# Kernel tuning notes

Hardware: AMD Instinct MI355X
Metric: run time of the kernel (lower is better)

Reference implementation:

```python
import jax, jax.numpy as jnp
import numpy as np

H = 2048          # hidden_size
I = 768           # moe_intermediate_size
E = 64            # num_experts
TOP_K = 8         # num_experts_per_tok (norm_topk_prob=True)
B, S = 1, 1024


def setup_inputs() -> dict:
    key = jax.random.key(0)
    ks = jax.random.split(key, 5)
    scale = 0.02
    return {
        "hidden_states": jax.random.normal(ks[0], (B, S, H), dtype=jnp.float32),
        "W_router": jax.random.normal(ks[1], (H, E), dtype=jnp.float32) * scale,
        "W_gate": jax.random.normal(ks[2], (E, H, I), dtype=jnp.float32) * scale,
        "W_up": jax.random.normal(ks[3], (E, H, I), dtype=jnp.float32) * scale,
        "W_down": jax.random.normal(ks[4], (E, I, H), dtype=jnp.float32) * scale,
    }


def reference(hidden_states, W_router, W_gate, W_up, W_down):
    b, s, h = hidden_states.shape
    x = hidden_states.reshape(-1, h)                      # [T, H]

    # --- Qwen3MoeTopKRouter: linear gate -> fp32 softmax -> top-k -> renorm ---
    logits = x @ W_router                                 # [T, E]
    probs = jax.nn.softmax(logits.astype(jnp.float32), axis=-1)
    top_w, top_idx = jax.lax.top_k(probs, TOP_K)          # [T, K]
    top_w = top_w / jnp.sum(top_w, axis=-1, keepdims=True)  # norm_topk_prob
    top_w = top_w.astype(x.dtype)

    # combine weights per (token, expert): zero if expert not selected
    comb = jnp.sum(jax.nn.one_hot(top_idx, E, dtype=x.dtype) * top_w[..., None], axis=1)  # [T, E]

    # --- per-expert SwiGLU MLP: down(silu(gate(x)) * up(x)), dense-masked ---
    g = jnp.einsum('th,ehi->eti', x, W_gate)              # [E, T, I]
    u = jnp.einsum('th,ehi->eti', x, W_up)                # [E, T, I]
    hmid = jax.nn.silu(g) * u                             # [E, T, I]
    # fold combine weight into the intermediate to avoid an [E, T, H] buffer
    hmid = hmid * comb.T[:, :, None]                      # [E, T, I]
    out = jnp.einsum('eti,eih->th', hmid, W_down)         # [T, H]

    return out.reshape(b, s, h)
```

## Files before the change

### kernel.cpp

```cpp
#include <hip/hip_runtime.h>
#include <hip/hip_bf16.h>

#define H_DIM 2048
#define I_DIM 768
#define NEXP 64
#define TOPK 8
#define NTOK 1024
#define BM 256
#define BKS 32

typedef float f32x4 __attribute__((ext_vector_type(4)));
typedef unsigned int u32x4 __attribute__((ext_vector_type(4)));
typedef unsigned int u32x2 __attribute__((ext_vector_type(2)));
typedef short bf16v8 __attribute__((ext_vector_type(8)));
typedef unsigned short u16x8 __attribute__((ext_vector_type(8)));
typedef unsigned int u32;

#define NTLOAD __builtin_nontemporal_load

#define WS_NEEDED 50954752ull

__device__ inline unsigned short f2bf(float f) {
    union { float f; u32 u; } v; v.f = f;
    u32 r = (v.u + 0x7FFFu + ((v.u >> 16) & 1u)) >> 16;
    return (unsigned short)r;
}
__device__ inline u32 pack2(float a, float b) {
    return (u32)f2bf(a) | ((u32)f2bf(b) << 16);
}

__global__ void zero_kernel(float4* p, int n4) {
    int i = blockIdx.x * blockDim.x + threadIdx.x;
    if (i < n4) p[i] = (float4){0.f, 0.f, 0.f, 0.f};
}

__global__ __launch_bounds__(512) void router_kernel(
    const float* __restrict__ x, const float* __restrict__ Wr,
    int* __restrict__ topk_idx, float* __restrict__ topk_w,
    ushort4* __restrict__ xbf)
{
    const int t   = blockIdx.x;
    const int tid = threadIdx.x;
    const int lane = tid & 63;
    const int wv   = tid >> 6;
    __shared__ float xs[H_DIM];
    __shared__ float red[8][64];

    const float* xrow = x + (size_t)t * H_DIM;
    {
        const float4* src = (const float4*)xrow;
        float4 v = src[tid];
        ((float4*)xs)[tid] = v;
        ushort4 o;
        o.x = f2bf(v.x); o.y = f2bf(v.y); o.z = f2bf(v.z); o.w = f2bf(v.w);
        xbf[(size_t)t * (H_DIM / 4) + tid] = o;
    }
    __syncthreads();

    float acc = 0.f;
    const int h0 = wv * 256;
    #pragma unroll 8
    for (int h = h0; h < h0 + 256; ++h) acc += xs[h] * Wr[(size_t)h * NEXP + lane];
    red[wv][lane] = acc;
    __syncthreads();

    if (tid < 64) {
        const int e = tid;
        float logit = ((red[0][e] + red[1][e]) + (red[2][e] + red[3][e]))
                    + ((red[4][e] + red[5][e]) + (red[6][e] + red[7][e]));

        float m = logit;
        #pragma unroll
        for (int o = 32; o > 0; o >>= 1) m = fmaxf(m, __shfl_xor(m, o));
        float p = __expf(logit - m);
        float s = p;
        #pragma unroll
        for (int o = 32; o > 0; o >>= 1) s += __shfl_xor(s, o);
        float prob = p / s;

        float myp = prob;
        float kw[TOPK]; int kid[TOPK]; float wsum = 0.f;
        #pragma unroll
        for (int k = 0; k < TOPK; ++k) {
            float v = myp; int bi = e;
            #pragma unroll
            for (int o = 32; o > 0; o >>= 1) {
                float ov = __shfl_xor(v, o);
                int   oi = __shfl_xor(bi, o);
                if (ov > v || (ov == v && oi < bi)) { v = ov; bi = oi; }
            }
            kw[k] = v; kid[k] = bi; wsum += v;
            if (e == bi) myp = -1.f;
        }
        if (e == 0) {
            float inv = 1.f / wsum;
            #pragma unroll
            for (int k = 0; k < TOPK; ++k) {
                topk_idx[t * TOPK + k] = kid[k];
                topk_w[t * TOPK + k]   = kw[k] * inv;
            }
        }
    }
}

__global__ __launch_bounds__(64) void listbuild_kernel(
    const int* __restrict__ topk_idx, const float* __restrict__ topk_w,
    int* __restrict__ counts, int* __restrict__ lists, float* __restrict__ wlist,
    int* __restrict__ invmap)
{
    const int e = blockIdx.x;
    const int lane = threadIdx.x;
    int n = 0;
    for (int base = 0; base < NTOK * TOPK; base += 64) {
        int s = base + lane;
        int idx = topk_idx[s];
        bool match = (idx == e);
        unsigned long long mask = __ballot(match);
        int pre = __popcll(mask & ((1ull << lane) - 1ull));
        if (match) {
            lists[e * NTOK + n + pre] = s >> 3;
            wlist[e * NTOK + n + pre] = topk_w[s];
            invmap[s] = n + pre;
        }
        n += __popcll(mask);
    }
    if (lane == 0) counts[e] = n;
}

__global__ __launch_bounds__(64) void scan_kernel(
    const int* __restrict__ counts, int* __restrict__ offsets)
{
    int e = threadIdx.x;
    int v = counts[e];
    int xacc = v;
    #pragma unroll
    for (int o = 1; o < 64; o <<= 1) {
        int y = __shfl_up(xacc, o);
        if (e >= o) xacc += y;
    }
    offsets[e] = xacc - v;
}

#define MFMA_BF16 __builtin_amdgcn_mfma_f32_16x16x32_bf16
#define LGKM0()  asm volatile("s_waitcnt lgkmcnt(0)" ::: "memory")
#define RAWBAR() __builtin_amdgcn_s_barrier()

__global__ __launch_bounds__(512) void gateup_kernel(
    const unsigned short* __restrict__ xbf,
    const float* __restrict__ Wg, const float* __restrict__ Wu,
    const int* __restrict__ counts, const int* __restrict__ offsets,
    const int* __restrict__ lists, const float* __restrict__ wlist,
    unsigned short* __restrict__ hmid)
{
    const int b  = blockIdx.x;
    const int wg = (b & 7) * 192 + (b >> 3);
    const int itile = wg % 24;
    const int e     = wg / 24;

    const int count = counts[e];
    if (count == 0) return;
    const int off = offsets[e];
    const int i0 = itile * 32;

    __shared__ unsigned short Alds[2][BM][40];
    __shared__ u32 Bgl[2][32 * 20];
    __shared__ u32 Bul[2][32 * 20];

    const int tid  = threadIdx.x;
    const int lane = tid & 63;
    const int wid  = tid >> 6;
    const int wm   = wid >> 1, wn = wid & 1;
    const int kb   = lane >> 4;
    const int l15  = lane & 15;

    const int ar = tid >> 1;
    const int ah = (tid & 1) * 16;
    const int bnn  = tid & 31;
    const int bkq  = (tid >> 5) & 7;
    const int bmat = tid >> 8;
    const float* WB = (bmat ? Wu : Wg) + (size_t)e * H_DIM * I_DIM + i0 + bnn;
    const int key4w = 4 * ((bnn >> 3) & 3);
    const int bwoff = bnn * 20 + ((2 * bkq) ^ key4w);
    const int brn   = wn * 16 + l15;
    const int key4r = 4 * ((brn >> 3) & 3);

    for (int mstart = 0; mstart < count; mstart += BM) {
        const int pr = mstart + ar;
        const bool aact = pr < count;
        const unsigned short* xrow = xbf + (size_t)(aact ? lists[e * NTOK + pr] : 0) * H_DIM + ah;
        const bool mact = (mstart + wm * 64) < count;

        f32x4 accg[4], accu[4];
        #pragma unroll
        for (int i = 0; i < 4; ++i) {
            accg[i] = (f32x4){0.f, 0.f, 0.f, 0.f};
            accu[i] = (f32x4){0.f, 0.f, 0.f, 0.f};
        }

        u32x4 aA0, aA1, aB0, aB1;
        float bA0, bA1, bA2, bA3;
        float bB0, bB1, bB2, bB3;

#define GU_LOADA(P0,P1,h)                                                       \
        if (aact) {                                                             \
            const u32x4* pa_ = (const u32x4*)(xrow + (h));                      \
            P0 = pa_[0]; P1 = pa_[1];                                           \
        }
#define GU_LOADB(R0,R1,R2,R3,h)                                                 \
        {                                                                       \
            R0 = NTLOAD(WB + (size_t)((h) + 4 * bkq)     * I_DIM);              \
            R1 = NTLOAD(WB + (size_t)((h) + 4 * bkq + 1) * I_DIM);              \
            R2 = NTLOAD(WB + (size_t)((h) + 4 * bkq + 2) * I_DIM);              \
            R3 = NTLOAD(WB + (size_t)((h) + 4 * bkq + 3) * I_DIM);              \
        }
#define GU_STORE(BUF,P0,P1,R0,R1,R2,R3)                                         \
        if (aact) {                                                             \
            *(u32x4*)&Alds[BUF][ar][ah]     = P0;                               \
            *(u32x4*)&Alds[BUF][ar][ah + 8] = P1;                               \
        }                                                                       \
        {                                                                       \
            u32x2 w_; w_.x = pack2(R0, R1); w_.y = pack2(R2, R3);               \
            *(u32x2*)((bmat ? Bul[BUF] : Bgl[BUF]) + bwoff) = w_;               \
        }
#define GU_MFMA(BUF)                                                            \
        if (mact) {                                                             \
            bf16v8 af[4], bg, bu;                                               \
            _Pragma("unroll")                                                   \
            for (int mf = 0; mf < 4; ++mf)                                      \
                af[mf] = *(const bf16v8*)&Alds[BUF][wm * 64 + mf * 16 + l15][kb * 8]; \
            bg = *(const bf16v8*)&Bgl[BUF][brn * 20 + ((4 * kb) ^ key4r)];      \
            bu = *(const bf16v8*)&Bul[BUF][brn * 20 + ((4 * kb) ^ key4r)];      \
            _Pragma("unroll")                                                   \
            for (int mf = 0; mf < 4; ++mf) {                                    \
                accg[mf] = MFMA_BF16(af[mf], bg, accg[mf], 0, 0, 0);            \
                accu[mf] = MFMA_BF16(af[mf], bu, accu[mf], 0, 0, 0);            \
            }                                                                   \
        }
#define GU_PHASE(BUF,P0,P1,R0,R1,R2,R3,nh)                                      \
        GU_STORE(BUF, P0, P1, R0, R1, R2, R3);                                  \
        if ((nh) < H_DIM) { GU_LOADB(R0, R1, R2, R3, (nh)); GU_LOADA(P0, P1, (nh)); } \
        LGKM0();                                                                \
        RAWBAR();                                                               \
        __builtin_amdgcn_s_setprio(1);                                          \
        GU_MFMA(BUF);                                                           \
        __builtin_amdgcn_s_setprio(0);

        GU_LOADB(bA0, bA1, bA2, bA3, 0);    GU_LOADA(aA0, aA1, 0);
        GU_LOADB(bB0, bB1, bB2, bB3, BKS);  GU_LOADA(aB0, aB1, BKS);

        for (int hh = 0; hh < H_DIM; hh += 2 * BKS) {
            GU_PHASE(0, aA0, aA1, bA0, bA1, bA2, bA3, hh + 2 * BKS);
            GU_PHASE(1, aB0, aB1, bB0, bB1, bB2, bB3, hh + 3 * BKS);
        }
        __syncthreads();
#undef GU_LOADA
#undef GU_LOADB
#undef GU_STORE
#undef GU_MFMA
#undef GU_PHASE

        if (mact) {
            #pragma unroll
            for (int mf = 0; mf < 4; ++mf)
                #pragma unroll
                for (int r = 0; r < 4; ++r) {
                    int pos = mstart + wm * 64 + mf * 16 + kb * 4 + r;
                    if (pos < count) {
                        float wgt = wlist[e * NTOK + pos];
                        float g = accg[mf][r], u = accu[mf][r];
                        float s = 1.f / (1.f + __expf(-g));
                        hmid[(size_t)(off + pos) * I_DIM + i0 + wn * 16 + l15] = f2bf(g * s * u * wgt);
                    }
                }
        }
    }
}

template <bool USE_PART>
__global__ __launch_bounds__(512) void down_kernel(
    const unsigned short* __restrict__ hmid, const float* __restrict__ Wd,
    const int* __restrict__ counts, const int* __restrict__ offsets,
    const int* __restrict__ lists, float* __restrict__ out,
    unsigned short* __restrict__ part)
{
    const int b  = blockIdx.x;
    const int wg = (b & 7) * 512 + (b >> 3);
    const int htile = wg % 64;
    const int e     = wg / 64;

    const int count = counts[e];
    if (count == 0) return;
    const int off = offsets[e];
    const int h0 = htile * 32;

    __shared__ unsigned short Alds[2][BM][40];
    __shared__ u32 Bdl[2][32 * 20];

    const int tid  = threadIdx.x;
    const int lane = tid & 63;
    const int wid  = tid >> 6;
    const int wm   = wid >> 1, wn = wid & 1;
    const int kb   = lane >> 4;
    const int l15  = lane & 15;

    const int ar = tid >> 1;
    const int ah = (tid & 1) * 16;
    const int bnn  = tid & 31;
    const int bkq  = (tid >> 5) & 7;
    const bool bact = tid < 256;
    const float* WB = Wd + (size_t)e * I_DIM * H_DIM + h0 + bnn;
    const int key4w = 4 * ((bnn >> 3) & 3);
    const int bwoff = bnn * 20 + ((2 * bkq) ^ key4w);
    const int brn   = wn * 16 + l15;
    const int key4r = 4 * ((brn >> 3) & 3);

    for (int mstart = 0; mstart < count; mstart += BM) {
        const int pr = mstart + ar;
        const bool aact = pr < count;
        const unsigned short* hrow = hmid + (size_t)(off + (aact ? pr : 0)) * I_DIM + ah;
        const bool mact = (mstart + wm * 64) < count;

        f32x4 acc[4];
        #pragma unroll
        for (int i = 0; i < 4; ++i) acc[i] = (f32x4){0.f, 0.f, 0.f, 0.f};

        u32x4 aA0, aA1, aB0, aB1;
        float bA0, bA1, bA2, bA3;
        float bB0, bB1, bB2, bB3;

#define DN_LOADA(P0,P1,k)                                                       \
        if (aact) {                                                             \
            const u32x4* p_ = (const u32x4*)(hrow + (k));                       \
            P0 = p_[0]; P1 = p_[1];                                             \
        }
#define DN_LOADB(R0,R1,R2,R3,k)                                                 \
        if (bact) {                                                             \
            R0 = NTLOAD(WB + (size_t)((k) + 4 * bkq)     * H_DIM);              \
            R1 = NTLOAD(WB + (size_t)((k) + 4 * bkq + 1) * H_DIM);              \
            R2 = NTLOAD(WB + (size_t)((k) + 4 * bkq + 2) * H_DIM);              \
            R3 = NTLOAD(WB + (size_t)((k) + 4 * bkq + 3) * H_DIM);              \
        }
#define DN_STORE(BUF,P0,P1,R0,R1,R2,R3)                                         \
        if (aact) {                                                             \
            *(u32x4*)&Alds[BUF][ar][ah]     = P0;                               \
            *(u32x4*)&Alds[BUF][ar][ah + 8] = P1;                               \
        }                                                                       \
        if (bact) {                                                             \
            u32x2 w_; w_.x = pack2(R0, R1); w_.y = pack2(R2, R3);               \
            *(u32x2*)(Bdl[BUF] + bwoff) = w_;                                   \
        }
#define DN_MFMA(BUF)                                                            \
        if (mact) {                                                             \
            bf16v8 af[4], bd;                                                   \
            _Pragma("unroll")                                                   \
            for (int mf = 0; mf < 4; ++mf)                                      \
                af[mf] = *(const bf16v8*)&Alds[BUF][wm * 64 + mf * 16 + l15][kb * 8]; \
            bd = *(const bf16v8*)&Bdl[BUF][brn * 20 + ((4 * kb) ^ key4r)];      \
            _Pragma("unroll")                                                   \
            for (int mf = 0; mf < 4; ++mf)                                      \
                acc[mf] = MFMA_BF16(af[mf], bd, acc[mf], 0, 0, 0);              \
        }
#define DN_PHASE(BUF,P0,P1,R0,R1,R2,R3,nk)                                      \
        DN_STORE(BUF, P0, P1, R0, R1, R2, R3);                                  \
        if ((nk) < I_DIM) { DN_LOADB(R0, R1, R2, R3, (nk)); DN_LOADA(P0, P1, (nk)); } \
        LGKM0();                                                                \
        RAWBAR();                                                               \
        __builtin_amdgcn_s_setprio(1);                                          \
        DN_MFMA(BUF);                                                           \
        __builtin_amdgcn_s_setprio(0);

        DN_LOADB(bA0, bA1, bA2, bA3, 0);    DN_LOADA(aA0, aA1, 0);
        DN_LOADB(bB0, bB1, bB2, bB3, BKS);  DN_LOADA(aB0, aB1, BKS);

        for (int ii = 0; ii < I_DIM; ii += 2 * BKS) {
            DN_PHASE(0, aA0, aA1, bA0, bA1, bA2, bA3, ii + 2 * BKS);
            DN_PHASE(1, aB0, aB1, bB0, bB1, bB2, bB3, ii + 3 * BKS);
        }
        __syncthreads();
#undef DN_LOADA
#undef DN_LOADB
#undef DN_STORE
#undef DN_MFMA
#undef DN_PHASE

        if (mact) {
            #pragma unroll
            for (int mf = 0; mf < 4; ++mf)
                #pragma unroll
                for (int r = 0; r < 4; ++r) {
                    int pos = mstart + wm * 64 + mf * 16 + kb * 4 + r;
                    if (pos < count) {
                        if constexpr (USE_PART) {
                            part[(size_t)(off + pos) * H_DIM + h0 + wn * 16 + l15] =
                                f2bf(acc[mf][r]);
                        } else {
                            int tok = lists[e * NTOK + pos];
                            atomicAdd(&out[(size_t)tok * H_DIM + h0 + wn * 16 + l15],
                                      acc[mf][r]);
                        }
                    }
                }
        }
    }
}

__global__ __launch_bounds__(256) void reduce_kernel(
    const unsigned short* __restrict__ part,
    const int* __restrict__ topk_idx, const int* __restrict__ invmap,
    const int* __restrict__ offsets, float* __restrict__ out)
{
    const int t   = blockIdx.x;
    const int tid = threadIdx.x;
    __shared__ int slots[TOPK];
    if (tid < TOPK) {
        int s = t * TOPK + tid;
        slots[tid] = offsets[topk_idx[s]] + invmap[s];
    }
    __syncthreads();

    const int c = tid * 8;
    float acc[8] = {0.f, 0.f, 0.f, 0.f, 0.f, 0.f, 0.f, 0.f};
    #pragma unroll
    for (int k = 0; k < TOPK; ++k) {
        u16x8 v = *(const u16x8*)&part[(size_t)slots[k] * H_DIM + c];
        #pragma unroll
        for (int j = 0; j < 8; ++j)
            acc[j] += __uint_as_float((u32)(unsigned short)v[j] << 16);
    }
    float4* dst = (float4*)&out[(size_t)t * H_DIM + c];
    dst[0] = (float4){acc[0], acc[1], acc[2], acc[3]};
    dst[1] = (float4){acc[4], acc[5], acc[6], acc[7]};
}

extern "C" void kernel_launch(void* const* d_in, const int* in_sizes, int n_in,
                              void* d_out, int out_size, void* d_ws, size_t ws_size,
                              hipStream_t stream) {
    const float* x  = (const float*)d_in[0];
    const float* Wr = (const float*)d_in[1];
    const float* Wg = (const float*)d_in[2];
    const float* Wu = (const float*)d_in[3];
    const float* Wd = (const float*)d_in[4];
    float* out = (float*)d_out;

    char* ws = (char*)d_ws;
    int*   topk_idx = (int*)  (ws + 0);
    float* topk_w   = (float*)(ws + 32768);
    int*   counts   = (int*)  (ws + 65536);
    int*   offsets  = (int*)  (ws + 65792);
    int*   lists    = (int*)  (ws + 66048);
    float* wlist    = (float*)(ws + 328192);
    int*   invmap   = (int*)  (ws + 590336);
    unsigned short* hmid = (unsigned short*)(ws + 623104);
    unsigned short* xbf  = (unsigned short*)(ws + 13206016);
    unsigned short* part = (unsigned short*)(ws + 17400320);

    const bool usePart = ws_size >= WS_NEEDED;

    hipLaunchKernelGGL(router_kernel, dim3(NTOK), dim3(512), 0, stream,
                       x, Wr, topk_idx, topk_w, (ushort4*)xbf);
    hipLaunchKernelGGL(listbuild_kernel, dim3(NEXP), dim3(64), 0, stream,
                       topk_idx, topk_w, counts, lists, wlist, invmap);
    hipLaunchKernelGGL(scan_kernel, dim3(1), dim3(64), 0, stream,
                       counts, offsets);
    hipLaunchKernelGGL(gateup_kernel, dim3(24 * NEXP), dim3(512), 0, stream,
                       xbf, Wg, Wu, counts, offsets, lists, wlist, hmid);
    if (usePart) {
        hipLaunchKernelGGL((down_kernel<true>), dim3(64 * NEXP), dim3(512), 0, stream,
                           hmid, Wd, counts, offsets, lists, out, part);
        hipLaunchKernelGGL(reduce_kernel, dim3(NTOK), dim3(256), 0, stream,
                           part, topk_idx, invmap, offsets, out);
    } else {
        const int nout4 = NTOK * H_DIM / 4;
        hipLaunchKernelGGL(zero_kernel, dim3((nout4 + 255) / 256), dim3(256), 0, stream,
                           (float4*)out, nout4);
        hipLaunchKernelGGL((down_kernel<false>), dim3(64 * NEXP), dim3(512), 0, stream,
                           hmid, Wd, counts, offsets, lists, out, part);
    }
}
```

Baseline: 472.1 us.

## Load activation tiles directly to LDS via global_load_lds with XOR swizzle

After: 479.2 us. About the same (+1.5%).

```diff
diff --git a/kernel.cpp b/kernel.cpp
--- a/kernel.cpp
+++ b/kernel.cpp
@@ -27,6 +27,12 @@
 }
 __device__ inline u32 pack2(float a, float b) {
     return (u32)f2bf(a) | ((u32)f2bf(b) << 16);
+}
+
+__device__ inline void async16(void* l, const void* g) {
+    __builtin_amdgcn_global_load_lds(
+        (const __attribute__((address_space(1))) unsigned int*)g,
+        (__attribute__((address_space(3))) unsigned int*)l, 16, 0, 0);
 }
 
 __global__ void zero_kernel(float4* p, int n4) {
@@ -144,6 +150,9 @@
 #define MFMA_BF16 __builtin_amdgcn_mfma_f32_16x16x32_bf16
 #define LGKM0()  asm volatile("s_waitcnt lgkmcnt(0)" ::: "memory")
 #define RAWBAR() __builtin_amdgcn_s_barrier()
+#define VMCNT4() asm volatile("s_waitcnt vmcnt(4)" ::: "memory")
+#define VMCNT0() asm volatile("s_waitcnt vmcnt(0)" ::: "memory")
+#define FENCE()  asm volatile("" ::: "memory")
 
 __global__ __launch_bounds__(512) void gateup_kernel(
     const unsigned short* __restrict__ xbf,
@@ -162,7 +171,7 @@
     const int off = offsets[e];
     const int i0 = itile * 32;
 
-    __shared__ unsigned short Alds[2][BM][40];
+    __shared__ unsigned short Alds[2][BM][32];
     __shared__ u32 Bgl[2][32 * 20];
     __shared__ u32 Bul[2][32 * 20];
 
@@ -173,8 +182,6 @@
     const int kb   = lane >> 4;
     const int l15  = lane & 15;
 
-    const int ar = tid >> 1;
-    const int ah = (tid & 1) * 16;
     const int bnn  = tid & 31;
     const int bkq  = (tid >> 5) & 7;
     const int bmat = tid >> 8;
@@ -184,10 +191,20 @@
     const int brn   = wn * 16 + l15;
     const int key4r = 4 * ((brn >> 3) & 3);
 
+    const int c4  = lane & 3;
+    const int r0  = wid * 32 + (lane >> 2);
+    const int r1  = r0 + 16;
+    const int awr0 = wid * 32;
+    const int awr1 = wid * 32 + 16;
+    const int aoff = (wm * 64 + l15) * 32 + ((kb ^ ((l15 >> 1) & 3)) * 8);
+
     for (int mstart = 0; mstart < count; mstart += BM) {
-        const int pr = mstart + ar;
-        const bool aact = pr < count;
-        const unsigned short* xrow = xbf + (size_t)(aact ? lists[e * NTOK + pr] : 0) * H_DIM + ah;
+        int p0 = mstart + r0; if (p0 >= count) p0 = count - 1;
+        int p1 = mstart + r1; if (p1 >= count) p1 = count - 1;
+        const unsigned short* srcA0 = xbf + (size_t)lists[e * NTOK + p0] * H_DIM
+                                      + (size_t)((c4 ^ ((r0 >> 1) & 3)) * 8);
+        const unsigned short* srcA1 = xbf + (size_t)lists[e * NTOK + p1] * H_DIM
+                                      + (size_t)((c4 ^ ((r1 >> 1) & 3)) * 8);
         const bool mact = (mstart + wm * 64) < count;
 
         f32x4 accg[4], accu[4];
@@ -197,15 +214,9 @@
             accu[i] = (f32x4){0.f, 0.f, 0.f, 0.f};
         }
 
-        u32x4 aA0, aA1, aB0, aB1;
         float bA0, bA1, bA2, bA3;
         float bB0, bB1, bB2, bB3;
 
-#define GU_LOADA(P0,P1,h)                                                       \
-        if (aact) {                                                             \
-            const u32x4* pa_ = (const u32x4*)(xrow + (h));                      \
-            P0 = pa_[0]; P1 = pa_[1];                                           \
-        }
 #define GU_LOADB(R0,R1,R2,R3,h)                                                 \
         {                                                                       \
             R0 = NTLOAD(WB + (size_t)((h) + 4 * bkq)     * I_DIM);              \
@@ -213,21 +224,23 @@
             R2 = NTLOAD(WB + (size_t)((h) + 4 * bkq + 2) * I_DIM);              \
             R3 = NTLOAD(WB + (size_t)((h) + 4 * bkq + 3) * I_DIM);              \
         }
-#define GU_STORE(BUF,P0,P1,R0,R1,R2,R3)                                         \
-        if (aact) {                                                             \
-            *(u32x4*)&Alds[BUF][ar][ah]     = P0;                               \
-            *(u32x4*)&Alds[BUF][ar][ah + 8] = P1;                               \
-        }                                                                       \
+#define GU_STOREB(BUF,R0,R1,R2,R3)                                              \
         {                                                                       \
             u32x2 w_; w_.x = pack2(R0, R1); w_.y = pack2(R2, R3);               \
             *(u32x2*)((bmat ? Bul[BUF] : Bgl[BUF]) + bwoff) = w_;               \
         }
+#define GU_DMAA(BUF,h)                                                          \
+        {                                                                       \
+            async16((void*)&Alds[BUF][awr0][0], (const void*)(srcA0 + (h)));    \
+            async16((void*)&Alds[BUF][awr1][0], (const void*)(srcA1 + (h)));    \
+        }
 #define GU_MFMA(BUF)                                                            \
         if (mact) {                                                             \
+            const unsigned short* Ab_ = (const unsigned short*)Alds[BUF];       \
             bf16v8 af[4], bg, bu;                                               \
             _Pragma("unroll")                                                   \
             for (int mf = 0; mf < 4; ++mf)                                      \
-                af[mf] = *(const bf16v8*)&Alds[BUF][wm * 64 + mf * 16 + l15][kb * 8]; \
+                af[mf] = *(const bf16v8*)&Ab_[aoff + mf * 512];                 \
             bg = *(const bf16v8*)&Bgl[BUF][brn * 20 + ((4 * kb) ^ key4r)];      \
             bu = *(const bf16v8*)&Bul[BUF][brn * 20 + ((4 * kb) ^ key4r)];      \
             _Pragma("unroll")                                                   \
@@ -236,26 +249,33 @@
                 accu[mf] = MFMA_BF16(af[mf], bu, accu[mf], 0, 0, 0);            \
             }                                                                   \
         }
-#define GU_PHASE(BUF,P0,P1,R0,R1,R2,R3,nh)                                      \
-        GU_STORE(BUF, P0, P1, R0, R1, R2, R3);                                  \
-        if ((nh) < H_DIM) { GU_LOADB(R0, R1, R2, R3, (nh)); GU_LOADA(P0, P1, (nh)); } \
+#define GU_PHASE(BUF,OBUF,R0,R1,R2,R3,nhB,nhA,VM)                               \
+        GU_STOREB(BUF, R0, R1, R2, R3);                                         \
+        if ((nhB) < H_DIM) GU_LOADB(R0, R1, R2, R3, (nhB));                     \
+        VM();                                                                   \
         LGKM0();                                                                \
         RAWBAR();                                                               \
+        FENCE();                                                                \
+        if ((nhA) < H_DIM) GU_DMAA(OBUF, (nhA));                                \
+        FENCE();                                                                \
         __builtin_amdgcn_s_setprio(1);                                          \
         GU_MFMA(BUF);                                                           \
         __builtin_amdgcn_s_setprio(0);
 
-        GU_LOADB(bA0, bA1, bA2, bA3, 0);    GU_LOADA(aA0, aA1, 0);
-        GU_LOADB(bB0, bB1, bB2, bB3, BKS);  GU_LOADA(aB0, aB1, BKS);
-
-        for (int hh = 0; hh < H_DIM; hh += 2 * BKS) {
-            GU_PHASE(0, aA0, aA1, bA0, bA1, bA2, bA3, hh + 2 * BKS);
-            GU_PHASE(1, aB0, aB1, bB0, bB1, bB2, bB3, hh + 3 * BKS);
-        }
+        GU_LOADB(bA0, bA1, bA2, bA3, 0);
+        GU_LOADB(bB0, bB1, bB2, bB3, BKS);
+        GU_DMAA(0, 0);
+
+        for (int hh = 0; hh < H_DIM - 2 * BKS; hh += 2 * BKS) {
+            GU_PHASE(0, 1, bA0, bA1, bA2, bA3, hh + 2 * BKS, hh + BKS,     VMCNT4);
+            GU_PHASE(1, 0, bB0, bB1, bB2, bB3, hh + 3 * BKS, hh + 2 * BKS, VMCNT4);
+        }
+        GU_PHASE(0, 1, bA0, bA1, bA2, bA3, H_DIM, H_DIM - BKS, VMCNT0);
+        GU_PHASE(1, 0, bB0, bB1, bB2, bB3, H_DIM, H_DIM,       VMCNT0);
         __syncthreads();
-#undef GU_LOADA
 #undef GU_LOADB
-#undef GU_STORE
+#undef GU_STOREB
+#undef GU_DMAA
 #undef GU_MFMA
 #undef GU_PHASE
 
@@ -293,7 +313,7 @@
     const int off = offsets[e];
     const int h0 = htile * 32;
 
-    __shared__ unsigned short Alds[2][BM][40];
+    __shared__ unsigned short Alds[2][BM][32];
     __shared__ u32 Bdl[2][32 * 20];
 
     const int tid  = threadIdx.x;
@@ -303,8 +323,6 @@
     const int kb   = lane >> 4;
     const int l15  = lane & 15;
 
-    const int ar = tid >> 1;
-    const int ah = (tid & 1) * 16;
     const int bnn  = tid & 31;
     const int bkq  = (tid >> 5) & 7;
     const bool bact = tid < 256;
@@ -314,25 +332,29 @@
     const int brn   = wn * 16 + l15;
     const int key4r = 4 * ((brn >> 3) & 3);
 
+    const int c4  = lane & 3;
+    const int r0  = wid * 32 + (lane >> 2);
+    const int r1  = r0 + 16;
+    const int awr0 = wid * 32;
+    const int awr1 = wid * 32 + 16;
+    const int aoff = (wm * 64 + l15) * 32 + ((kb ^ ((l15 >> 1) & 3)) * 8);
+
     for (int mstart = 0; mstart < count; mstart += BM) {
-        const int pr = mstart + ar;
-        const bool aact = pr < count;
-        const unsigned short* hrow = hmid + (size_t)(off + (aact ? pr : 0)) * I_DIM + ah;
+        int p0 = mstart + r0; if (p0 >= count) p0 = count - 1;
+        int p1 = mstart + r1; if (p1 >= count) p1 = count - 1;
+        const unsigned short* srcA0 = hmid + (size_t)(off + p0) * I_DIM
+                                      + (size_t)((c4 ^ ((r0 >> 1) & 3)) * 8);
+        const unsigned short* srcA1 = hmid + (size_t)(off + p1) * I_DIM
+                                      + (size_t)((c4 ^ ((r1 >> 1) & 3)) * 8);
         const bool mact = (mstart + wm * 64) < count;
 
         f32x4 acc[4];
         #pragma unroll
         for (int i = 0; i < 4; ++i) acc[i] = (f32x4){0.f, 0.f, 0.f, 0.f};
 
-        u32x4 aA0, aA1, aB0, aB1;
         float bA0, bA1, bA2, bA3;
         float bB0, bB1, bB2, bB3;
 
-#define DN_LOADA(P0,P1,k)                                                       \
-        if (aact) {                                                             \
-            const u32x4* p_ = (const u32x4*)(hrow + (k));                       \
-            P0 = p_[0]; P1 = p_[1];                                             \
-        }
 #define DN_LOADB(R0,R1,R2,R3,k)                                                 \
         if (bact) {                                                             \
             R0 = NTLOAD(WB + (size_t)((k) + 4 * bkq)     * H_DIM);              \
@@ -340,47 +362,60 @@
             R2 = NTLOAD(WB + (size_t)((k) + 4 * bkq + 2) * H_DIM);              \
             R3 = NTLOAD(WB + (size_t)((k) + 4 * bkq + 3) * H_DIM);              \
         }
-#define DN_STORE(BUF,P0,P1,R0,R1,R2,R3)                                         \
-        if (aact) {                                                             \
-            *(u32x4*)&Alds[BUF][ar][ah]     = P0;                               \
-            *(u32x4*)&Alds[BUF][ar][ah + 8] = P1;                               \
-        }                                                                       \
+#define DN_STOREB(BUF,R0,R1,R2,R3)                                              \
         if (bact) {                                                             \
             u32x2 w_; w_.x = pack2(R0, R1); w_.y = pack2(R2, R3);               \
             *(u32x2*)(Bdl[BUF] + bwoff) = w_;                                   \
         }
+#define DN_DMAA(BUF,k)                                                          \
+        {                                                                       \
+            async16((void*)&Alds[BUF][awr0][0], (const void*)(srcA0 + (k)));    \
+            async16((void*)&Alds[BUF][awr1][0], (const void*)(srcA1 + (k)));    \
+        }
 #define DN_MFMA(BUF)                                                            \
         if (mact) {                                                             \
+            const unsigned short* Ab_ = (const unsigned short*)Alds[BUF];       \
             bf16v8 af[4], bd;                                                   \
             _Pragma("unroll")                                                   \
             for (int mf = 0; mf < 4; ++mf)                                      \
-                af[mf] = *(const bf16v8*)&Alds[BUF][wm * 64 + mf * 16 + l15][kb * 8]; \
+                af[mf] = *(const bf16v8*)&Ab_[aoff + mf * 512];                 \
             bd = *(const bf16v8*)&Bdl[BUF][brn * 20 + ((4 * kb) ^ key4r)];      \
             _Pragma("unroll")                                                   \
             for (int mf = 0; mf < 4; ++mf)                                      \
                 acc[mf] = MFMA_BF16(af[mf], bd, acc[mf], 0, 0, 0);              \
         }
-#define DN_PHASE(BUF,P0,P1,R0,R1,R2,R3,nk)                                      \
-        DN_STORE(BUF, P0, P1, R0, R1, R2, R3);                                  \
-        if ((nk) < I_DIM) { DN_LOADB(R0, R1, R2, R3, (nk)); DN_LOADA(P0, P1, (nk)); } \
+#define DN_VMS()  { if (bact) { VMCNT4(); } else { VMCNT0(); } }
+#define DN_VMT()  VMCNT0()
+#define DN_PHASE(BUF,OBUF,R0,R1,R2,R3,nkB,nkA,VM)                               \
+        DN_STOREB(BUF, R0, R1, R2, R3);                                         \
+        if ((nkB) < I_DIM) DN_LOADB(R0, R1, R2, R3, (nkB));                     \
+        VM();                                                                   \
         LGKM0();                                                                \
         RAWBAR();                                                               \
+        FENCE();                                                                \
+        if ((nkA) < I_DIM) DN_DMAA(OBUF, (nkA));                                \
+        FENCE();                                                                \
         __builtin_amdgcn_s_setprio(1);                                          \
         DN_MFMA(BUF);                                                           \
         __builtin_amdgcn_s_setprio(0);
 
-        DN_LOADB(bA0, bA1, bA2, bA3, 0);    DN_LOADA(aA0, aA1, 0);
-        DN_LOADB(bB0, bB1, bB2, bB3, BKS);  DN_LOADA(aB0, aB1, BKS);
-
-        for (int ii = 0; ii < I_DIM; ii += 2 * BKS) {
-            DN_PHASE(0, aA0, aA1, bA0, bA1, bA2, bA3, ii + 2 * BKS);
-            DN_PHASE(1, aB0, aB1, bB0, bB1, bB2, bB3, ii + 3 * BKS);
-        }
+        DN_LOADB(bA0, bA1, bA2, bA3, 0);
+        DN_LOADB(bB0, bB1, bB2, bB3, BKS);
+        DN_DMAA(0, 0);
+
+        for (int ii = 0; ii < I_DIM - 2 * BKS; ii += 2 * BKS) {
+            DN_PHASE(0, 1, bA0, bA1, bA2, bA3, ii + 2 * BKS, ii + BKS,     DN_VMS);
+            DN_PHASE(1, 0, bB0, bB1, bB2, bB3, ii + 3 * BKS, ii + 2 * BKS, DN_VMS);
+        }
+        DN_PHASE(0, 1, bA0, bA1, bA2, bA3, I_DIM, I_DIM - BKS, DN_VMT);
+        DN_PHASE(1, 0, bB0, bB1, bB2, bB3, I_DIM, I_DIM,       DN_VMT);
         __syncthreads();
-#undef DN_LOADA
 #undef DN_LOADB
-#undef DN_STORE
+#undef DN_STOREB
+#undef DN_DMAA
 #undef DN_MFMA
+#undef DN_VMS
+#undef DN_VMT
 #undef DN_PHASE
 
         if (mact) {
```
